# Performance work log

Hardware: AMD Instinct MI355X
Metric: run time of the kernel (lower is better)

Reference implementation:

```python
import jax, jax.numpy as jnp
import numpy as np

MARGIN = 0.0
BINS = 10
ALPHA = 0.75
N = 16777216  # number of ranking pairs


def setup_inputs() -> dict:
    key = jax.random.key(0)
    k1, k2, k3 = jax.random.split(key, 3)
    output1 = jax.random.normal(k1, (N,), dtype=jnp.float32)
    output2 = jax.random.normal(k2, (N,), dtype=jnp.float32)
    # MarginRankingLoss targets are -1 or +1
    t = jax.random.randint(k3, (N,), 0, 2)
    target = (2 * t - 1).astype(jnp.float32)
    return {"output1": output1, "output2": output2, "target": target}


def reference(output1, output2, target):
    # MarginRankingLoss(reduction='none'): max(0, -target*(x1-x2) + margin)
    diff = output1 - output2
    loss = jnp.maximum(0.0, -target * diff + MARGIN)
    # gradient-norm proxy: g = sigmoid(-diff * (2*target - 1) + margin)
    expected_sign = 2.0 * target - 1.0
    g = jax.nn.sigmoid(-diff * expected_sign + MARGIN)
    # histogram binning over |g| with uniform edges [i/bins, (i+1)/bins)
    # (g is a sigmoid output so |g| == g); floor(g*bins) reproduces the
    # torch per-bin boolean-mask loop in a single pass
    bin_idx = jnp.clip(jnp.floor(g * BINS).astype(jnp.int32), 0, BINS - 1)
    tot = jax.ops.segment_sum(jnp.ones_like(g), bin_idx, num_segments=BINS)
    tot = jnp.maximum(tot, 1.0)  # clamp(min=1)
    w = tot ** (-ALPHA)
    # counts come from .item() in torch -> detached from autograd
    sample_weights = jax.lax.stop_gradient(w[bin_idx])
    return (loss * sample_weights).mean()
```

## Files before the change

### kernel.cpp

```cpp
#include <hip/hip_runtime.h>
#include <math.h>

#define NBINS 10
#define ALPHA 0.75f


__device__ __forceinline__ void ghm_process(float x1, float x2, float t,
                                            float* __restrict__ s,
                                            unsigned int* __restrict__ c) {
    float diff = x1 - x2;
    float loss = fmaxf(0.0f, -t * diff);
    float es   = 2.0f * t - 1.0f;
    float x    = -diff * es;
    float g    = 1.0f / (1.0f + __expf(-x));
    int bin    = (int)floorf(g * 10.0f);
    bin = min(max(bin, 0), NBINS - 1);
#pragma unroll
    for (int b = 0; b < NBINS; ++b) {
        bool m = (bin == b);
        s[b] += m ? loss : 0.0f;
        c[b] += m ? 1u : 0u;
    }
}

__global__ __launch_bounds__(256) void ghm_hist_kernel(
        const float* __restrict__ o1, const float* __restrict__ o2,
        const float* __restrict__ tg,
        float* __restrict__ g_sums, unsigned int* __restrict__ g_counts,
        int n) {
    float s[NBINS];
    unsigned int c[NBINS];
#pragma unroll
    for (int b = 0; b < NBINS; ++b) { s[b] = 0.0f; c[b] = 0u; }

    const int n4 = n >> 2;
    const float4* __restrict__ v1 = (const float4*)o1;
    const float4* __restrict__ v2 = (const float4*)o2;
    const float4* __restrict__ vt = (const float4*)tg;

    const int idx    = blockIdx.x * blockDim.x + threadIdx.x;
    const int stride = gridDim.x * blockDim.x;

    for (int i = idx; i < n4; i += stride) {
        float4 a = v1[i];
        float4 b = v2[i];
        float4 t = vt[i];
        ghm_process(a.x, b.x, t.x, s, c);
        ghm_process(a.y, b.y, t.y, s, c);
        ghm_process(a.z, b.z, t.z, s, c);
        ghm_process(a.w, b.w, t.w, s, c);
    }
    const int tail_base = n4 << 2;
    const int tail = n - tail_base;
    if (idx < tail) {
        ghm_process(o1[tail_base + idx], o2[tail_base + idx], tg[tail_base + idx], s, c);
    }

#pragma unroll
    for (int b = 0; b < NBINS; ++b) {
        float sv = s[b];
        unsigned int cv = c[b];
#pragma unroll
        for (int off = 32; off > 0; off >>= 1) {
            sv += __shfl_down(sv, off, 64);
            cv += __shfl_down(cv, off, 64);
        }
        s[b] = sv;
        c[b] = cv;
    }

    __shared__ float        ls[4][NBINS];
    __shared__ unsigned int lc[4][NBINS];
    const int wave = threadIdx.x >> 6;
    const int lane = threadIdx.x & 63;
    if (lane == 0) {
#pragma unroll
        for (int b = 0; b < NBINS; ++b) { ls[wave][b] = s[b]; lc[wave][b] = c[b]; }
    }
    __syncthreads();
    if (threadIdx.x < NBINS) {
        float sv = 0.0f;
        unsigned int cv = 0u;
#pragma unroll
        for (int w = 0; w < 4; ++w) { sv += ls[w][threadIdx.x]; cv += lc[w][threadIdx.x]; }
        atomicAdd(&g_sums[threadIdx.x], sv);
        atomicAdd(&g_counts[threadIdx.x], cv);
    }
}

__global__ void ghm_final_kernel(const float* __restrict__ g_sums,
                                 const unsigned int* __restrict__ g_counts,
                                 float* __restrict__ out, float inv_n) {
    if (threadIdx.x == 0 && blockIdx.x == 0) {
        float acc = 0.0f;
#pragma unroll
        for (int b = 0; b < NBINS; ++b) {
            float tot = fmaxf((float)g_counts[b], 1.0f);
            float w = powf(tot, -ALPHA);
            acc += g_sums[b] * w;
        }
        out[0] = acc * inv_n;
    }
}

extern "C" void kernel_launch(void* const* d_in, const int* in_sizes, int n_in,
                              void* d_out, int out_size, void* d_ws, size_t ws_size,
                              hipStream_t stream) {
    const float* o1 = (const float*)d_in[0];
    const float* o2 = (const float*)d_in[1];
    const float* tg = (const float*)d_in[2];
    float* out = (float*)d_out;
    const int n = in_sizes[0];

    float* g_sums = (float*)d_ws;
    unsigned int* g_counts = (unsigned int*)((char*)d_ws + NBINS * sizeof(float));

    hipMemsetAsync(d_ws, 0, NBINS * (sizeof(float) + sizeof(unsigned int)), stream);

    const int block = 256;
    int grid = (n / 4 + block - 1) / block;
    if (grid > 2048) grid = 2048;

    ghm_hist_kernel<<<grid, block, 0, stream>>>(o1, o2, tg, g_sums, g_counts, n);
    ghm_final_kernel<<<1, 64, 0, stream>>>(g_sums, g_counts, out, 1.0f / (float)n);
}
```

Before: 225.3 us.

## Replace sigmoid binning with logit-threshold cumulative counts and unroll loads

Drops the exp/reciprocal sigmoid and bin index computation. Each element's logit x is compared against nine precomputed logit thresholds to build cumulative (>=) counts, and loss is accumulated cumulatively for only the upper five bins, since loss is zero whenever x < 0. Per-bin counts and sums are recovered by differencing in the final kernel. The main loop also loads two float4 strides per iteration to raise memory-level parallelism. The risk is that the logit thresholds can put edge cases in a different bin than the original sigmoid-then-floor path, and differencing float cumulative sums can add rounding error.

```diff
diff --git a/kernel.cpp b/kernel.cpp
--- a/kernel.cpp
+++ b/kernel.cpp
@@ -5,33 +5,35 @@
 #define ALPHA 0.75f
 
 
-__device__ __forceinline__ void ghm_process(float x1, float x2, float t,
-                                            float* __restrict__ s,
-                                            unsigned int* __restrict__ c) {
+__device__ __forceinline__ void ghm_elem(float x1, float x2, float t,
+                                         unsigned int* __restrict__ cc,
+                                         float* __restrict__ ss) {
+    const float L[9] = {-2.19722458f, -1.38629436f, -0.84729786f, -0.40546511f,
+                         0.0f,         0.40546511f,  0.84729786f,  1.38629436f,
+                         2.19722458f};
     float diff = x1 - x2;
+    float es   = __builtin_fmaf(2.0f, t, -1.0f);
+    float x    = -diff * es;
     float loss = fmaxf(0.0f, -t * diff);
-    float es   = 2.0f * t - 1.0f;
-    float x    = -diff * es;
-    float g    = 1.0f / (1.0f + __expf(-x));
-    int bin    = (int)floorf(g * 10.0f);
-    bin = min(max(bin, 0), NBINS - 1);
 #pragma unroll
-    for (int b = 0; b < NBINS; ++b) {
-        bool m = (bin == b);
-        s[b] += m ? loss : 0.0f;
-        c[b] += m ? 1u : 0u;
-    }
+    for (int k = 0; k < 9; ++k)
+        cc[k] += (x >= L[k]) ? 1u : 0u;
+#pragma unroll
+    for (int j = 0; j < 5; ++j)
+        ss[j] += (x >= L[4 + j]) ? loss : 0.0f;
 }
 
 __global__ __launch_bounds__(256) void ghm_hist_kernel(
         const float* __restrict__ o1, const float* __restrict__ o2,
         const float* __restrict__ tg,
-        float* __restrict__ g_sums, unsigned int* __restrict__ g_counts,
+        unsigned int* __restrict__ g_cc, float* __restrict__ g_ss,
         int n) {
-    float s[NBINS];
-    unsigned int c[NBINS];
+    unsigned int cc[9];
+    float ss[5];
 #pragma unroll
-    for (int b = 0; b < NBINS; ++b) { s[b] = 0.0f; c[b] = 0u; }
+    for (int k = 0; k < 9; ++k) cc[k] = 0u;
+#pragma unroll
+    for (int j = 0; j < 5; ++j) ss[j] = 0.0f;
 
     const int n4 = n >> 2;
     const float4* __restrict__ v1 = (const float4*)o1;
@@ -41,65 +43,97 @@
     const int idx    = blockIdx.x * blockDim.x + threadIdx.x;
     const int stride = gridDim.x * blockDim.x;
 
-    for (int i = idx; i < n4; i += stride) {
-        float4 a = v1[i];
-        float4 b = v2[i];
-        float4 t = vt[i];
-        ghm_process(a.x, b.x, t.x, s, c);
-        ghm_process(a.y, b.y, t.y, s, c);
-        ghm_process(a.z, b.z, t.z, s, c);
-        ghm_process(a.w, b.w, t.w, s, c);
+    int i = idx;
+    for (; i + stride < n4; i += 2 * stride) {
+        float4 a0 = v1[i];
+        float4 b0 = v2[i];
+        float4 t0 = vt[i];
+        float4 a1 = v1[i + stride];
+        float4 b1 = v2[i + stride];
+        float4 t1 = vt[i + stride];
+        ghm_elem(a0.x, b0.x, t0.x, cc, ss);
+        ghm_elem(a0.y, b0.y, t0.y, cc, ss);
+        ghm_elem(a0.z, b0.z, t0.z, cc, ss);
+        ghm_elem(a0.w, b0.w, t0.w, cc, ss);
+        ghm_elem(a1.x, b1.x, t1.x, cc, ss);
+        ghm_elem(a1.y, b1.y, t1.y, cc, ss);
+        ghm_elem(a1.z, b1.z, t1.z, cc, ss);
+        ghm_elem(a1.w, b1.w, t1.w, cc, ss);
+    }
+    for (; i < n4; i += stride) {
+        float4 a0 = v1[i];
+        float4 b0 = v2[i];
+        float4 t0 = vt[i];
+        ghm_elem(a0.x, b0.x, t0.x, cc, ss);
+        ghm_elem(a0.y, b0.y, t0.y, cc, ss);
+        ghm_elem(a0.z, b0.z, t0.z, cc, ss);
+        ghm_elem(a0.w, b0.w, t0.w, cc, ss);
     }
     const int tail_base = n4 << 2;
-    const int tail = n - tail_base;
-    if (idx < tail) {
-        ghm_process(o1[tail_base + idx], o2[tail_base + idx], tg[tail_base + idx], s, c);
+    if (idx < n - tail_base) {
+        ghm_elem(o1[tail_base + idx], o2[tail_base + idx], tg[tail_base + idx], cc, ss);
     }
 
 #pragma unroll
-    for (int b = 0; b < NBINS; ++b) {
-        float sv = s[b];
-        unsigned int cv = c[b];
+    for (int k = 0; k < 9; ++k) {
+        unsigned int v = cc[k];
 #pragma unroll
-        for (int off = 32; off > 0; off >>= 1) {
-            sv += __shfl_down(sv, off, 64);
-            cv += __shfl_down(cv, off, 64);
-        }
-        s[b] = sv;
-        c[b] = cv;
+        for (int off = 32; off > 0; off >>= 1) v += __shfl_down(v, off, 64);
+        cc[k] = v;
+    }
+#pragma unroll
+    for (int j = 0; j < 5; ++j) {
+        float v = ss[j];
+#pragma unroll
+        for (int off = 32; off > 0; off >>= 1) v += __shfl_down(v, off, 64);
+        ss[j] = v;
     }
 
-    __shared__ float        ls[4][NBINS];
-    __shared__ unsigned int lc[4][NBINS];
+    __shared__ unsigned int lc[4][9];
+    __shared__ float        ls[4][5];
     const int wave = threadIdx.x >> 6;
     const int lane = threadIdx.x & 63;
     if (lane == 0) {
 #pragma unroll
-        for (int b = 0; b < NBINS; ++b) { ls[wave][b] = s[b]; lc[wave][b] = c[b]; }
+        for (int k = 0; k < 9; ++k) lc[wave][k] = cc[k];
+#pragma unroll
+        for (int j = 0; j < 5; ++j) ls[wave][j] = ss[j];
     }
     __syncthreads();
-    if (threadIdx.x < NBINS) {
-        float sv = 0.0f;
-        unsigned int cv = 0u;
+    if (threadIdx.x < 9) {
+        unsigned int v = 0u;
 #pragma unroll
-        for (int w = 0; w < 4; ++w) { sv += ls[w][threadIdx.x]; cv += lc[w][threadIdx.x]; }
-        atomicAdd(&g_sums[threadIdx.x], sv);
-        atomicAdd(&g_counts[threadIdx.x], cv);
+        for (int w = 0; w < 4; ++w) v += lc[w][threadIdx.x];
+        atomicAdd(&g_cc[threadIdx.x], v);
+    } else if (threadIdx.x >= 16 && threadIdx.x < 21) {
+        const int j = threadIdx.x - 16;
+        float v = 0.0f;
+#pragma unroll
+        for (int w = 0; w < 4; ++w) v += ls[w][j];
+        atomicAdd(&g_ss[j], v);
     }
 }
 
-__global__ void ghm_final_kernel(const float* __restrict__ g_sums,
-                                 const unsigned int* __restrict__ g_counts,
-                                 float* __restrict__ out, float inv_n) {
+__global__ void ghm_final_kernel(const unsigned int* __restrict__ g_cc,
+                                 const float* __restrict__ g_ss,
+                                 float* __restrict__ out, int n) {
     if (threadIdx.x == 0 && blockIdx.x == 0) {
+        float tot[NBINS];
+        tot[0] = (float)(n - (int)g_cc[0]);
+#pragma unroll
+        for (int b = 1; b < 9; ++b) tot[b] = (float)(g_cc[b - 1] - g_cc[b]);
+        tot[9] = (float)g_cc[8];
+        float s[5];
+#pragma unroll
+        for (int j = 0; j < 4; ++j) s[j] = g_ss[j] - g_ss[j + 1];
+        s[4] = g_ss[4];
         float acc = 0.0f;
 #pragma unroll
-        for (int b = 0; b < NBINS; ++b) {
-            float tot = fmaxf((float)g_counts[b], 1.0f);
-            float w = powf(tot, -ALPHA);
-            acc += g_sums[b] * w;
+        for (int j = 0; j < 5; ++j) {
+            float t = fmaxf(tot[5 + j], 1.0f);
+            acc += s[j] * powf(t, -ALPHA);
         }
-        out[0] = acc * inv_n;
+        out[0] = acc / (float)n;
     }
 }
 
@@ -112,15 +146,15 @@
     float* out = (float*)d_out;
     const int n = in_sizes[0];
 
-    float* g_sums = (float*)d_ws;
-    unsigned int* g_counts = (unsigned int*)((char*)d_ws + NBINS * sizeof(float));
+    unsigned int* g_cc = (unsigned int*)d_ws;
+    float* g_ss = (float*)((char*)d_ws + 16 * sizeof(unsigned int));
 
-    hipMemsetAsync(d_ws, 0, NBINS * (sizeof(float) + sizeof(unsigned int)), stream);
+    hipMemsetAsync(d_ws, 0, 32 * sizeof(unsigned int), stream);
 
     const int block = 256;
     int grid = (n / 4 + block - 1) / block;
     if (grid > 2048) grid = 2048;
 
-    ghm_hist_kernel<<<grid, block, 0, stream>>>(o1, o2, tg, g_sums, g_counts, n);
-    ghm_final_kernel<<<1, 64, 0, stream>>>(g_sums, g_counts, out, 1.0f / (float)n);
+    ghm_hist_kernel<<<grid, block, 0, stream>>>(o1, o2, tg, g_cc, g_ss, n);
+    ghm_final_kernel<<<1, 64, 0, stream>>>(g_cc, g_ss, out, n);
 }
```

Result: faster. 207.7 us (-7.8%).

## Replace sigmoid binning with logit thresholds and cumulative 5-bin counts

Applied to the files above, without the earlier changes.

The sigmoid and floor binning are replaced by comparisons of the pre-sigmoid logit against the logit of each bin edge. Per-bin values become cumulative counts and loss sums over the upper five bins, and the final kernel recovers them by differencing. The lower five bins are dropped because, with ±1 targets, the hinge loss is zero whenever the logit is negative. The main loop also gains a two-stage register double-buffer for the float4 loads. This removes the exp, the reciprocal and half of the per-element select work, but relies on targets being exactly ±1 and may differ from the reference on floating-point results that land exactly on a bin edge.

```diff
diff --git a/kernel.cpp b/kernel.cpp
--- a/kernel.cpp
+++ b/kernel.cpp
@@ -1,105 +1,130 @@
 #include <hip/hip_runtime.h>
 #include <math.h>
 
-#define NBINS 10
 #define ALPHA 0.75f
 
-
-__device__ __forceinline__ void ghm_process(float x1, float x2, float t,
-                                            float* __restrict__ s,
-                                            unsigned int* __restrict__ c) {
-    float diff = x1 - x2;
-    float loss = fmaxf(0.0f, -t * diff);
-    float es   = 2.0f * t - 1.0f;
-    float x    = -diff * es;
-    float g    = 1.0f / (1.0f + __expf(-x));
-    int bin    = (int)floorf(g * 10.0f);
-    bin = min(max(bin, 0), NBINS - 1);
-#pragma unroll
-    for (int b = 0; b < NBINS; ++b) {
-        bool m = (bin == b);
-        s[b] += m ? loss : 0.0f;
-        c[b] += m ? 1u : 0u;
-    }
-}
+#define L5 0.0f
+#define L6 0.40546510810816444f
+#define L7 0.8472978603872037f
+#define L8 1.3862943611198906f
+#define L9 2.1972245773362196f
 
 __global__ __launch_bounds__(256) void ghm_hist_kernel(
+        const float4* __restrict__ v1, const float4* __restrict__ v2,
+        const float4* __restrict__ vt,
         const float* __restrict__ o1, const float* __restrict__ o2,
         const float* __restrict__ tg,
-        float* __restrict__ g_sums, unsigned int* __restrict__ g_counts,
+        unsigned int* __restrict__ g_cc, float* __restrict__ g_ss,
         int n) {
-    float s[NBINS];
-    unsigned int c[NBINS];
-#pragma unroll
-    for (int b = 0; b < NBINS; ++b) { s[b] = 0.0f; c[b] = 0u; }
+    unsigned int cc0 = 0, cc1 = 0, cc2 = 0, cc3 = 0, cc4 = 0;
+    float        ss0 = 0, ss1 = 0, ss2 = 0, ss3 = 0, ss4 = 0;
 
-    const int n4 = n >> 2;
-    const float4* __restrict__ v1 = (const float4*)o1;
-    const float4* __restrict__ v2 = (const float4*)o2;
-    const float4* __restrict__ vt = (const float4*)tg;
+    auto elem = [&](float x1, float x2, float t) {
+        float diff = x1 - x2;
+        float es   = __builtin_fmaf(2.0f, t, -1.0f);
+        float x    = -diff * es;
+        float loss = fmaxf(0.0f, -t * diff);
+        cc0 += (x >= L5);  ss0 += (x >= L5) ? loss : 0.0f;
+        cc1 += (x >= L6);  ss1 += (x >= L6) ? loss : 0.0f;
+        cc2 += (x >= L7);  ss2 += (x >= L7) ? loss : 0.0f;
+        cc3 += (x >= L8);  ss3 += (x >= L8) ? loss : 0.0f;
+        cc4 += (x >= L9);  ss4 += (x >= L9) ? loss : 0.0f;
+    };
+    auto quad = [&](const float4& a, const float4& b, const float4& t) {
+        elem(a.x, b.x, t.x); elem(a.y, b.y, t.y);
+        elem(a.z, b.z, t.z); elem(a.w, b.w, t.w);
+    };
 
+    const int n4     = n >> 2;
     const int idx    = blockIdx.x * blockDim.x + threadIdx.x;
     const int stride = gridDim.x * blockDim.x;
 
-    for (int i = idx; i < n4; i += stride) {
-        float4 a = v1[i];
-        float4 b = v2[i];
-        float4 t = vt[i];
-        ghm_process(a.x, b.x, t.x, s, c);
-        ghm_process(a.y, b.y, t.y, s, c);
-        ghm_process(a.z, b.z, t.z, s, c);
-        ghm_process(a.w, b.w, t.w, s, c);
-    }
-    const int tail_base = n4 << 2;
-    const int tail = n - tail_base;
-    if (idx < tail) {
-        ghm_process(o1[tail_base + idx], o2[tail_base + idx], tg[tail_base + idx], s, c);
+    if (idx < n4) {
+        const int K = 1 + (n4 - 1 - idx) / stride;
+        float4 Aa, Ab, At, Ba, Bb, Bt;
+        int i = idx;
+        Aa = v1[i]; Ab = v2[i]; At = vt[i];
+        int k = 0;
+        while (k + 2 <= K - 1) {
+            const int i1 = i + stride;
+            Ba = v1[i1]; Bb = v2[i1]; Bt = vt[i1];
+            quad(Aa, Ab, At);
+            const int i2 = i1 + stride;
+            Aa = v1[i2]; Ab = v2[i2]; At = vt[i2];
+            quad(Ba, Bb, Bt);
+            i = i2;
+            k += 2;
+        }
+        if (k < K - 1) {
+            const int i1 = i + stride;
+            Ba = v1[i1]; Bb = v2[i1]; Bt = vt[i1];
+            quad(Aa, Ab, At);
+            quad(Ba, Bb, Bt);
+        } else {
+            quad(Aa, Ab, At);
+        }
     }
 
+    const int tail_base = n4 << 2;
+    if (idx < n - tail_base) {
+        elem(o1[tail_base + idx], o2[tail_base + idx], tg[tail_base + idx]);
+    }
+
+    float sv[5] = {ss0, ss1, ss2, ss3, ss4};
+    unsigned int cv[5] = {cc0, cc1, cc2, cc3, cc4};
 #pragma unroll
-    for (int b = 0; b < NBINS; ++b) {
-        float sv = s[b];
-        unsigned int cv = c[b];
+    for (int q = 0; q < 5; ++q) {
+        unsigned int c = cv[q];
+        float        s = sv[q];
 #pragma unroll
         for (int off = 32; off > 0; off >>= 1) {
-            sv += __shfl_down(sv, off, 64);
-            cv += __shfl_down(cv, off, 64);
+            c += __shfl_down(c, off, 64);
+            s += __shfl_down(s, off, 64);
         }
-        s[b] = sv;
-        c[b] = cv;
+        cv[q] = c; sv[q] = s;
     }
 
-    __shared__ float        ls[4][NBINS];
-    __shared__ unsigned int lc[4][NBINS];
+    __shared__ unsigned int lc[4][5];
+    __shared__ float        ls[4][5];
     const int wave = threadIdx.x >> 6;
     const int lane = threadIdx.x & 63;
     if (lane == 0) {
 #pragma unroll
-        for (int b = 0; b < NBINS; ++b) { ls[wave][b] = s[b]; lc[wave][b] = c[b]; }
+        for (int q = 0; q < 5; ++q) { lc[wave][q] = cv[q]; ls[wave][q] = sv[q]; }
     }
     __syncthreads();
-    if (threadIdx.x < NBINS) {
-        float sv = 0.0f;
-        unsigned int cv = 0u;
+    if (threadIdx.x < 5) {
+        unsigned int c = 0u;
 #pragma unroll
-        for (int w = 0; w < 4; ++w) { sv += ls[w][threadIdx.x]; cv += lc[w][threadIdx.x]; }
-        atomicAdd(&g_sums[threadIdx.x], sv);
-        atomicAdd(&g_counts[threadIdx.x], cv);
+        for (int w = 0; w < 4; ++w) c += lc[w][threadIdx.x];
+        atomicAdd(&g_cc[threadIdx.x], c);
+    } else if (threadIdx.x >= 16 && threadIdx.x < 21) {
+        const int q = threadIdx.x - 16;
+        float s = 0.0f;
+#pragma unroll
+        for (int w = 0; w < 4; ++w) s += ls[w][q];
+        atomicAdd(&g_ss[q], s);
     }
 }
 
-__global__ void ghm_final_kernel(const float* __restrict__ g_sums,
-                                 const unsigned int* __restrict__ g_counts,
-                                 float* __restrict__ out, float inv_n) {
+__global__ void ghm_final_kernel(const unsigned int* __restrict__ g_cc,
+                                 const float* __restrict__ g_ss,
+                                 float* __restrict__ out, int n) {
     if (threadIdx.x == 0 && blockIdx.x == 0) {
+        float tot[5], s[5];
+#pragma unroll
+        for (int j = 0; j < 4; ++j) {
+            tot[j] = (float)(g_cc[j] - g_cc[j + 1]);
+            s[j]   = g_ss[j] - g_ss[j + 1];
+        }
+        tot[4] = (float)g_cc[4];
+        s[4]   = g_ss[4];
         float acc = 0.0f;
 #pragma unroll
-        for (int b = 0; b < NBINS; ++b) {
-            float tot = fmaxf((float)g_counts[b], 1.0f);
-            float w = powf(tot, -ALPHA);
-            acc += g_sums[b] * w;
+        for (int j = 0; j < 5; ++j) {
+            acc += s[j] * powf(fmaxf(tot[j], 1.0f), -ALPHA);
         }
-        out[0] = acc * inv_n;
+        out[0] = acc / (float)n;
     }
 }
 
@@ -112,15 +137,19 @@
     float* out = (float*)d_out;
     const int n = in_sizes[0];
 
-    float* g_sums = (float*)d_ws;
-    unsigned int* g_counts = (unsigned int*)((char*)d_ws + NBINS * sizeof(float));
+    unsigned int* g_cc = (unsigned int*)d_ws;
+    float* g_ss = (float*)((char*)d_ws + 8 * sizeof(unsigned int));
 
-    hipMemsetAsync(d_ws, 0, NBINS * (sizeof(float) + sizeof(unsigned int)), stream);
+    hipMemsetAsync(d_ws, 0, 16 * sizeof(unsigned int), stream);
 
     const int block = 256;
-    int grid = (n / 4 + block - 1) / block;
+    const int n4 = n >> 2;
+    int grid = (n4 + block - 1) / block;
+    if (grid < 1) grid = 1;
     if (grid > 2048) grid = 2048;
 
-    ghm_hist_kernel<<<grid, block, 0, stream>>>(o1, o2, tg, g_sums, g_counts, n);
-    ghm_final_kernel<<<1, 64, 0, stream>>>(g_sums, g_counts, out, 1.0f / (float)n);
+    ghm_hist_kernel<<<grid, block, 0, stream>>>(
+        (const float4*)o1, (const float4*)o2, (const float4*)tg,
+        o1, o2, tg, g_cc, g_ss, n);
+    ghm_final_kernel<<<1, 64, 0, stream>>>(g_cc, g_ss, out, n);
 }
```

Measured after the change: 215.9 us. -4.2%, faster.
